# Kernel tuning notes

Hardware: AMD Instinct MI355X
Metric: run time of the kernel (lower is better)

Reference implementation:

```python
import jax, jax.numpy as jnp
import numpy as np

B, T, D = 512, 200, 512

def setup_inputs() -> dict:
    key = jax.random.key(0)
    k1, k2, k3 = jax.random.split(key, 3)
    inputs = jax.random.normal(k1, (B, T, D), dtype=jnp.float32)
    # Keras 'uniform' initializer -> U(-0.05, 0.05)
    W = jax.random.uniform(k2, (T, T), minval=-0.05, maxval=0.05, dtype=jnp.float32)
    b = jax.random.uniform(k3, (T,), minval=-0.05, maxval=0.05, dtype=jnp.float32)
    return {"inputs": inputs, "W": W, "b": b}

def reference(inputs, W, b):
    # x = permute(inputs, (0,2,1)) -> [B, D, T]; scores over timestep axis
    # a = softmax(tanh(x @ W + b)) along last axis (T)
    scores = jnp.tanh(jnp.einsum('btd,ts->bds', inputs, W) + b)  # [B, D, T]
    a = jax.nn.softmax(scores, axis=-1)                           # softmax over T
    # permute back to [B, T, D], elementwise multiply, sum over T -> [B, D]
    out = jnp.einsum('bdt,btd->bd', a, inputs)
    return out
```

## Files before the change

### kernel.cpp

```cpp
#include <hip/hip_runtime.h>
#include <cstdint>
#include <cstddef>

#define B_DIM 512
#define T_DIM 200
#define D_DIM 512
#define NPAD  208
#define NKG   28
#define NT    13
#define DT    128
#define KS_STEPS 7

typedef short  short8  __attribute__((ext_vector_type(8)));
typedef float  floatx4 __attribute__((ext_vector_type(4)));

__device__ __forceinline__ unsigned short f2bf(float f) {
  unsigned int u = __float_as_uint(f);
  u += 0x7fffu + ((u >> 16) & 1u);
  return (unsigned short)(u >> 16);
}
__device__ __forceinline__ float bf2f(unsigned short h) {
  return __uint_as_float(((unsigned int)h) << 16);
}

__global__ void prep_w_kernel(const float* __restrict__ W,
                              unsigned short* __restrict__ wf) {
  int idx = blockIdx.x * blockDim.x + threadIdx.x;
  if (idx >= NKG * 8 * NPAD) return;
  int k = idx / NPAD;
  int n = idx - k * NPAD;
  float v = (k < T_DIM && n < T_DIM) ? W[k * T_DIM + n] : 0.0f;
  wf[((size_t)(k >> 3) * NPAD + n) * 8 + (k & 7)] = f2bf(v);
}

__global__ __launch_bounds__(256, 2)
void attn_kernel(const float* __restrict__ X,
                 const unsigned short* __restrict__ wf,
                 const float* __restrict__ bias,
                 float* __restrict__ out) {
  __shared__ unsigned short Xa[NKG * DT * 8];

  const int tid = threadIdx.x;
  const int bb  = blockIdx.x >> 2;
  const int d0  = (blockIdx.x & 3) * DT;

  {
    const int m    = tid & (DT - 1);
    const int half = tid >> 7;
    for (int kk = half; kk < NKG; kk += 2) {
      unsigned short pk[8];
      if (kk < 25) {
        const float* g = X + ((size_t)bb * T_DIM + (size_t)kk * 8) * D_DIM + d0 + m;
        #pragma unroll
        for (int j = 0; j < 8; ++j) pk[j] = f2bf(g[(size_t)j * D_DIM]);
      } else {
        #pragma unroll
        for (int j = 0; j < 8; ++j) pk[j] = 0;
      }
      int4 w;
      w.x = (int)pk[0] | ((int)pk[1] << 16);
      w.y = (int)pk[2] | ((int)pk[3] << 16);
      w.z = (int)pk[4] | ((int)pk[5] << 16);
      w.w = (int)pk[6] | ((int)pk[7] << 16);
      *(int4*)(&Xa[(kk * DT + m) * 8]) = w;
    }
  }
  __syncthreads();

  const int lane = tid & 63;
  const int l15  = lane & 15;
  const int g    = lane >> 4;
  const int wv   = tid >> 6;
  const int mt0  = wv * 2;

  float bv[NT];
  #pragma unroll
  for (int nt = 0; nt < NT; ++nt) {
    int n = nt * 16 + l15;
    bv[nt] = (n < T_DIM) ? bias[n] : 0.0f;
  }

  floatx4 acc[2][NT];
  #pragma unroll
  for (int mt = 0; mt < 2; ++mt)
    #pragma unroll
    for (int nt = 0; nt < NT; ++nt)
      acc[mt][nt] = (floatx4){0.f, 0.f, 0.f, 0.f};

  for (int ks = 0; ks < KS_STEPS; ++ks) {
    const int kg = ks * 4 + g;
    short8 a0 = *(const short8*)(&Xa[(kg * DT + mt0 * 16 + l15) * 8]);
    short8 a1 = *(const short8*)(&Xa[(kg * DT + mt0 * 16 + 16 + l15) * 8]);
    const unsigned short* wp = wf + ((size_t)kg * NPAD + l15) * 8;
    #pragma unroll
    for (int nt = 0; nt < NT; ++nt) {
      short8 bfr = *(const short8*)(wp + nt * 16 * 8);
      acc[0][nt] = __builtin_amdgcn_mfma_f32_16x16x32_bf16(a0, bfr, acc[0][nt], 0, 0, 0);
      acc[1][nt] = __builtin_amdgcn_mfma_f32_16x16x32_bf16(a1, bfr, acc[1][nt], 0, 0, 0);
    }
  }

  #pragma unroll
  for (int mt = 0; mt < 2; ++mt) {
    const int mtile = mt0 + mt;
    float sc[NT][4];
    float rmax[4] = {-3.0e38f, -3.0e38f, -3.0e38f, -3.0e38f};
    #pragma unroll
    for (int nt = 0; nt < NT; ++nt) {
      const int n = nt * 16 + l15;
      const bool valid = (n < T_DIM);
      #pragma unroll
      for (int r = 0; r < 4; ++r) {
        float s;
        if (valid) {
          float z = acc[mt][nt][r] + bv[nt];
          float e = __expf(2.0f * z);
          s = 1.0f - __fdividef(2.0f, e + 1.0f);
        } else {
          s = -1.0e30f;
        }
        sc[nt][r] = s;
        rmax[r] = fmaxf(rmax[r], s);
      }
    }
    #pragma unroll
    for (int off = 1; off <= 8; off <<= 1)
      #pragma unroll
      for (int r = 0; r < 4; ++r)
        rmax[r] = fmaxf(rmax[r], __shfl_xor(rmax[r], off, 64));

    float rsum[4] = {0.f, 0.f, 0.f, 0.f};
    #pragma unroll
    for (int nt = 0; nt < NT; ++nt)
      #pragma unroll
      for (int r = 0; r < 4; ++r) {
        float p = __expf(sc[nt][r] - rmax[r]);
        sc[nt][r] = p;
        rsum[r] += p;
      }
    #pragma unroll
    for (int off = 1; off <= 8; off <<= 1)
      #pragma unroll
      for (int r = 0; r < 4; ++r)
        rsum[r] += __shfl_xor(rsum[r], off, 64);

    float part[4] = {0.f, 0.f, 0.f, 0.f};
    #pragma unroll
    for (int nt = 0; nt < NT; ++nt) {
      const int t = nt * 16 + l15;
      const unsigned short* xp = &Xa[((t >> 3) * DT) * 8 + (t & 7)];
      #pragma unroll
      for (int r = 0; r < 4; ++r) {
        const int m = mtile * 16 + g * 4 + r;
        part[r] += sc[nt][r] * bf2f(xp[m * 8]);
      }
    }
    #pragma unroll
    for (int off = 1; off <= 8; off <<= 1)
      #pragma unroll
      for (int r = 0; r < 4; ++r)
        part[r] += __shfl_xor(part[r], off, 64);

    if (l15 == 0) {
      #pragma unroll
      for (int r = 0; r < 4; ++r)
        out[(size_t)bb * D_DIM + d0 + mtile * 16 + g * 4 + r] = part[r] * (1.0f / rsum[r]);
    }
  }
}

extern "C" void kernel_launch(void* const* d_in, const int* in_sizes, int n_in,
                              void* d_out, int out_size, void* d_ws, size_t ws_size,
                              hipStream_t stream) {
  const float* X  = (const float*)d_in[0];
  const float* W  = (const float*)d_in[1];
  const float* bs = (const float*)d_in[2];
  float* out = (float*)d_out;
  unsigned short* wf = (unsigned short*)d_ws;

  const int wtot = NKG * 8 * NPAD;
  hipLaunchKernelGGL(prep_w_kernel, dim3((wtot + 255) / 256), dim3(256), 0, stream,
                     W, wf);
  hipLaunchKernelGGL(attn_kernel, dim3(B_DIM * (D_DIM / DT)), dim3(256), 0, stream,
                     X, wf, bs, out);
}
```

Measured before the change: 372.0 us.

## Halve D tile, one M-tile per wave, fuse softmax without max pass

Shrinks the per-block D tile from 128 to 64 and doubles the grid, so each wave computes one 16-row M tile instead of two. This cuts accumulator registers and LDS, and launch bounds are raised to allow four blocks per CU. The softmax drops the running-max pass because tanh bounds scores to [-1,1], so exp, sum and the weighted accumulation happen in one fused loop. The loss is that W fragments are reused across only one A tile per wave, so global and L2 traffic for W grows.

```diff
diff --git a/kernel.cpp b/kernel.cpp
--- a/kernel.cpp
+++ b/kernel.cpp
@@ -8,7 +8,7 @@
 #define NPAD  208
 #define NKG   28
 #define NT    13
-#define DT    128
+#define DT    64
 #define KS_STEPS 7
 
 typedef short  short8  __attribute__((ext_vector_type(8)));
@@ -33,7 +33,7 @@
   wf[((size_t)(k >> 3) * NPAD + n) * 8 + (k & 7)] = f2bf(v);
 }
 
-__global__ __launch_bounds__(256, 2)
+__global__ __launch_bounds__(256, 4)
 void attn_kernel(const float* __restrict__ X,
                  const unsigned short* __restrict__ wf,
                  const float* __restrict__ bias,
@@ -41,13 +41,13 @@
   __shared__ unsigned short Xa[NKG * DT * 8];
 
   const int tid = threadIdx.x;
-  const int bb  = blockIdx.x >> 2;
-  const int d0  = (blockIdx.x & 3) * DT;
+  const int bb  = blockIdx.x >> 3;
+  const int d0  = (blockIdx.x & 7) * DT;
 
   {
-    const int m    = tid & (DT - 1);
-    const int half = tid >> 7;
-    for (int kk = half; kk < NKG; kk += 2) {
+    const int m = tid & (DT - 1);
+    const int q = tid >> 6;
+    for (int kk = q; kk < NKG; kk += 4) {
       unsigned short pk[8];
       if (kk < 25) {
         const float* g = X + ((size_t)bb * T_DIM + (size_t)kk * 8) * D_DIM + d0 + m;
@@ -71,7 +71,6 @@
   const int l15  = lane & 15;
   const int g    = lane >> 4;
   const int wv   = tid >> 6;
-  const int mt0  = wv * 2;
 
   float bv[NT];
   #pragma unroll
@@ -80,92 +79,54 @@
     bv[nt] = (n < T_DIM) ? bias[n] : 0.0f;
   }
 
-  floatx4 acc[2][NT];
+  floatx4 acc[NT];
   #pragma unroll
-  for (int mt = 0; mt < 2; ++mt)
-    #pragma unroll
-    for (int nt = 0; nt < NT; ++nt)
-      acc[mt][nt] = (floatx4){0.f, 0.f, 0.f, 0.f};
+  for (int nt = 0; nt < NT; ++nt)
+    acc[nt] = (floatx4){0.f, 0.f, 0.f, 0.f};
 
   for (int ks = 0; ks < KS_STEPS; ++ks) {
     const int kg = ks * 4 + g;
-    short8 a0 = *(const short8*)(&Xa[(kg * DT + mt0 * 16 + l15) * 8]);
-    short8 a1 = *(const short8*)(&Xa[(kg * DT + mt0 * 16 + 16 + l15) * 8]);
+    short8 a = *(const short8*)(&Xa[(kg * DT + wv * 16 + l15) * 8]);
     const unsigned short* wp = wf + ((size_t)kg * NPAD + l15) * 8;
     #pragma unroll
     for (int nt = 0; nt < NT; ++nt) {
       short8 bfr = *(const short8*)(wp + nt * 16 * 8);
-      acc[0][nt] = __builtin_amdgcn_mfma_f32_16x16x32_bf16(a0, bfr, acc[0][nt], 0, 0, 0);
-      acc[1][nt] = __builtin_amdgcn_mfma_f32_16x16x32_bf16(a1, bfr, acc[1][nt], 0, 0, 0);
+      acc[nt] = __builtin_amdgcn_mfma_f32_16x16x32_bf16(a, bfr, acc[nt], 0, 0, 0);
     }
   }
 
+  float part[4] = {0.f, 0.f, 0.f, 0.f};
+  float rs[4]   = {0.f, 0.f, 0.f, 0.f};
   #pragma unroll
-  for (int mt = 0; mt < 2; ++mt) {
-    const int mtile = mt0 + mt;
-    float sc[NT][4];
-    float rmax[4] = {-3.0e38f, -3.0e38f, -3.0e38f, -3.0e38f};
+  for (int nt = 0; nt < NT; ++nt) {
+    const int t = nt * 16 + l15;
+    const bool valid = (t < T_DIM);
+    const unsigned short* xp = &Xa[((t >> 3) * DT) * 8 + (t & 7)];
     #pragma unroll
-    for (int nt = 0; nt < NT; ++nt) {
-      const int n = nt * 16 + l15;
-      const bool valid = (n < T_DIM);
-      #pragma unroll
-      for (int r = 0; r < 4; ++r) {
-        float s;
-        if (valid) {
-          float z = acc[mt][nt][r] + bv[nt];
-          float e = __expf(2.0f * z);
-          s = 1.0f - __fdividef(2.0f, e + 1.0f);
-        } else {
-          s = -1.0e30f;
-        }
-        sc[nt][r] = s;
-        rmax[r] = fmaxf(rmax[r], s);
+    for (int r = 0; r < 4; ++r) {
+      if (valid) {
+        float z  = acc[nt][r] + bv[nt];
+        float e  = __expf(2.0f * z);
+        float th = 1.0f - __fdividef(2.0f, e + 1.0f);
+        float p  = __expf(th);
+        rs[r]   += p;
+        const int m = wv * 16 + g * 4 + r;
+        part[r] += p * bf2f(xp[m * 8]);
       }
     }
+  }
+  #pragma unroll
+  for (int off = 1; off <= 8; off <<= 1)
     #pragma unroll
-    for (int off = 1; off <= 8; off <<= 1)
-      #pragma unroll
-      for (int r = 0; r < 4; ++r)
-        rmax[r] = fmaxf(rmax[r], __shfl_xor(rmax[r], off, 64));
+    for (int r = 0; r < 4; ++r) {
+      part[r] += __shfl_xor(part[r], off, 16);
+      rs[r]   += __shfl_xor(rs[r],   off, 16);
+    }
 
-    float rsum[4] = {0.f, 0.f, 0.f, 0.f};
+  if (l15 == 0) {
     #pragma unroll
-    for (int nt = 0; nt < NT; ++nt)
-      #pragma unroll
-      for (int r = 0; r < 4; ++r) {
-        float p = __expf(sc[nt][r] - rmax[r]);
-        sc[nt][r] = p;
-        rsum[r] += p;
-      }
-    #pragma unroll
-    for (int off = 1; off <= 8; off <<= 1)
-      #pragma unroll
-      for (int r = 0; r < 4; ++r)
-        rsum[r] += __shfl_xor(rsum[r], off, 64);
-
-    float part[4] = {0.f, 0.f, 0.f, 0.f};
-    #pragma unroll
-    for (int nt = 0; nt < NT; ++nt) {
-      const int t = nt * 16 + l15;
-      const unsigned short* xp = &Xa[((t >> 3) * DT) * 8 + (t & 7)];
-      #pragma unroll
-      for (int r = 0; r < 4; ++r) {
-        const int m = mtile * 16 + g * 4 + r;
-        part[r] += sc[nt][r] * bf2f(xp[m * 8]);
-      }
-    }
-    #pragma unroll
-    for (int off = 1; off <= 8; off <<= 1)
-      #pragma unroll
-      for (int r = 0; r < 4; ++r)
-        part[r] += __shfl_xor(part[r], off, 64);
-
-    if (l15 == 0) {
-      #pragma unroll
-      for (int r = 0; r < 4; ++r)
-        out[(size_t)bb * D_DIM + d0 + mtile * 16 + g * 4 + r] = part[r] * (1.0f / rsum[r]);
-    }
+    for (int r = 0; r < 4; ++r)
+      out[(size_t)bb * D_DIM + d0 + wv * 16 + g * 4 + r] = part[r] * __frcp_rn(rs[r]);
   }
 }
 
```

New measurement: 347.5 us. -6.6%, faster.
